# Optimization experiments

Measured on AMD Instinct MI355X. Metric: run time of the kernel, lower is better.

The kernel has to match this reference:

```python
import jax, jax.numpy as jnp
import numpy as np

B, S, DIM = 1, 2048, 2048
NH, NKV, HD = 32, 8, 64
NREP = NH // NKV
SCALE = 1.0 / float(np.sqrt(HD))
NEG = -1e30


def _apply_rope(q, k, rope_cache):
    # q: (B,S,NH,HD), k: (B,S,NKV,HD); rope_cache: (S, HD) = [cos | sin], each HD//2 wide
    cos = rope_cache[:, : HD // 2][None, :, None, :]  # (1,S,1,HD/2)
    sin = rope_cache[:, HD // 2 :][None, :, None, :]

    def rot(x):
        x1, x2 = x[..., : HD // 2], x[..., HD // 2 :]
        return jnp.concatenate([x1 * cos - x2 * sin, x1 * sin + x2 * cos], axis=-1)

    return rot(q), rot(k)


def setup_inputs() -> dict:
    key = jax.random.key(0)
    ks = jax.random.split(key, 12)
    std = 0.02
    x = jax.random.normal(ks[0], (B, S, DIM), jnp.float32)
    # real rotary cos/sin cache
    inv_freq = 1.0 / (10000.0 ** (np.arange(0, HD, 2, dtype=np.float64) / HD))
    freqs = np.outer(np.arange(S, dtype=np.float64), inv_freq)
    rope_cache = jnp.asarray(
        np.concatenate([np.cos(freqs), np.sin(freqs)], axis=-1), jnp.float32
    )  # (S, HD)
    return {
        "x": x,
        "rope_cache": rope_cache,
        "wq_w": jax.random.normal(ks[1], (NH * HD, DIM), jnp.float32) * std,
        "wq_b": jax.random.normal(ks[2], (NH * HD,), jnp.float32) * std,
        "wk_w": jax.random.normal(ks[3], (NKV * HD, DIM), jnp.float32) * std,
        "wk_b": jax.random.normal(ks[4], (NKV * HD,), jnp.float32) * std,
        "wv_w": jax.random.normal(ks[5], (NKV * HD, DIM), jnp.float32) * std,
        "wv_b": jax.random.normal(ks[6], (NKV * HD,), jnp.float32) * std,
        "wo_w": jax.random.normal(ks[7], (DIM, NH * HD), jnp.float32) * std,
        "wo_b": jax.random.normal(ks[8], (DIM,), jnp.float32) * std,
        "sinks": jax.random.normal(ks[9], (NH,), jnp.float32) * std,
    }


def reference(x, rope_cache, wq_w, wq_b, wk_w, wk_b, wv_w, wv_b, wo_w, wo_b, sinks):
    q = (x @ wq_w.T + wq_b).reshape(B, S, NH, HD)
    k = (x @ wk_w.T + wk_b).reshape(B, S, NKV, HD)
    v = (x @ wv_w.T + wv_b).reshape(B, S, NKV, HD)
    q, k = _apply_rope(q, k, rope_cache)
    q = q.transpose(0, 2, 1, 3)  # (B,NH,S,HD)
    k = jnp.repeat(k.transpose(0, 2, 1, 3), NREP, axis=1)  # GQA expand -> (B,NH,S,HD)
    v = jnp.repeat(v.transpose(0, 2, 1, 3), NREP, axis=1)
    scores = jnp.einsum("bhqd,bhkd->bhqk", q, k) * SCALE
    causal = jnp.tril(jnp.ones((S, S), bool))
    scores = jnp.where(causal[None, None], scores, NEG)
    lse = jax.scipy.special.logsumexp(scores, axis=-1)  # (B,NH,S)
    attn = jnp.exp(scores - lse[..., None])
    out = jnp.einsum("bhqk,bhkd->bhqd", attn, v)
    sink_scale = jax.nn.sigmoid(lse - sinks[None, :, None])  # (B,NH,S)
    out = out * sink_scale[..., None]
    out = out.transpose(0, 2, 1, 3).reshape(B, S, NH * HD)
    return out @ wo_w.T + wo_b
```

## Files before the change

### kernel.cpp

```cpp
#include <hip/hip_runtime.h>

typedef unsigned short ushort_t;
typedef short s8v __attribute__((ext_vector_type(8)));
typedef short s4v __attribute__((ext_vector_type(4)));
typedef float f4v __attribute__((ext_vector_type(4)));

#define DIMK   2048
#define NHEAD  32
#define HDIM   64

__device__ __forceinline__ unsigned short f2bf(float f) {
    unsigned u = __float_as_uint(f);
    u += 0x7fffu + ((u >> 16) & 1u);
    return (unsigned short)(u >> 16);
}

__device__ __forceinline__ void gll16(const void* g, void* l) {
    __builtin_amdgcn_global_load_lds(
        (const __attribute__((address_space(1))) void*)g,
        (__attribute__((address_space(3))) void*)l, 16, 0, 0);
}

__device__ __forceinline__ f4v mfma16(s8v a, s8v b, f4v c) {
    return __builtin_amdgcn_mfma_f32_16x16x32_bf16(a, b, c, 0, 0, 0);
}

__global__ __launch_bounds__(256) void cast_all(
    const float* __restrict__ x,  const float* __restrict__ wq,
    const float* __restrict__ wk, const float* __restrict__ wv,
    const float* __restrict__ wo,
    ushort_t* __restrict__ xb,  ushort_t* __restrict__ wqb,
    ushort_t* __restrict__ wkb, ushort_t* __restrict__ wvb,
    ushort_t* __restrict__ wob)
{
    int i = blockIdx.x * 256 + threadIdx.x;
    const float* src; ushort_t* dst;
    if      (i < 1048576) { src = x;  dst = xb; }
    else if (i < 2097152) { src = wq; dst = wqb; i -= 1048576; }
    else if (i < 2359296) { src = wk; dst = wkb; i -= 2097152; }
    else if (i < 2621440) { src = wv; dst = wvb; i -= 2359296; }
    else                  { src = wo; dst = wob; i -= 2621440; }
    float4 v = ((const float4*)src)[i];
    ushort4 o;
    o.x = f2bf(v.x); o.y = f2bf(v.y); o.z = f2bf(v.z); o.w = f2bf(v.w);
    ((ushort4*)dst)[i] = o;
}

__device__ __forceinline__ void gemm_core(
    const ushort_t* __restrict__ A, const ushort_t* __restrict__ Bt,
    int bm, int bn, ushort_t* As, ushort_t* Bs, f4v acc[4][4])
{
    const int tid  = threadIdx.x;
    const int wave = tid >> 6, lane = tid & 63;
    const int c = lane & 15, q4 = lane >> 4;
    const int wm = (wave >> 1) * 64, wn = (wave & 1) * 64;

    const ushort_t* ag = A  + (size_t)(bm * 128 + wave * 32 + (lane >> 2)) * DIMK + (lane & 3) * 8;
    const ushort_t* bg = Bt + (size_t)(bn * 128 + wave * 32 + (lane >> 2)) * DIMK + (lane & 3) * 8;
    ushort_t* as0 = As + (wave * 32) * 32;
    ushort_t* as1 = As + (wave * 32 + 16) * 32;
    ushort_t* bs0 = Bs + (wave * 32) * 32;
    ushort_t* bs1 = Bs + (wave * 32 + 16) * 32;

    for (int k0 = 0; k0 < DIMK; k0 += 32) {
        gll16(ag + k0,             as0);
        gll16(ag + 16 * DIMK + k0, as1);
        gll16(bg + k0,             bs0);
        gll16(bg + 16 * DIMK + k0, bs1);
        __syncthreads();
        s8v af[4], bfv[4];
#pragma unroll
        for (int mt = 0; mt < 4; ++mt)
            af[mt] = *(const s8v*)(As + (wm + mt * 16 + c) * 32 + q4 * 8);
#pragma unroll
        for (int nt = 0; nt < 4; ++nt)
            bfv[nt] = *(const s8v*)(Bs + (wn + nt * 16 + c) * 32 + q4 * 8);
#pragma unroll
        for (int mt = 0; mt < 4; ++mt)
#pragma unroll
            for (int nt = 0; nt < 4; ++nt)
                acc[mt][nt] = mfma16(af[mt], bfv[nt], acc[mt][nt]);
        __syncthreads();
    }
}

__global__ __launch_bounds__(256) void qkv_gemm(
    const ushort_t* __restrict__ Xb,
    const ushort_t* __restrict__ Wqb, const ushort_t* __restrict__ Wkb, const ushort_t* __restrict__ Wvb,
    const float* __restrict__ biasq, const float* __restrict__ biask, const float* __restrict__ biasv,
    const float* __restrict__ rope,
    ushort_t* __restrict__ Qo, ushort_t* __restrict__ Kblk, ushort_t* __restrict__ Vblk)
{
    __shared__ ushort_t As[128 * 32], Bs[128 * 32];
    const int nb = blockIdx.x, bm = blockIdx.y;
    const ushort_t* Bt; const float* bias; int nbl, mode;
    if      (nb < 16) { Bt = Wqb; bias = biasq; nbl = nb;      mode = 0; }
    else if (nb < 20) { Bt = Wkb; bias = biask; nbl = nb - 16; mode = 1; }
    else              { Bt = Wvb; bias = biasv; nbl = nb - 20; mode = 2; }

    const f4v fz = {0.f, 0.f, 0.f, 0.f};
    f4v acc[4][4];
    for (int i = 0; i < 4; ++i) for (int j = 0; j < 4; ++j) acc[i][j] = fz;

    gemm_core(Xb, Bt, bm, nbl, As, Bs, acc);

    const int tid = threadIdx.x, wave = tid >> 6, lane = tid & 63;
    const int c = lane & 15, q4 = lane >> 4;
    const int wm = (wave >> 1) * 64, wn = (wave & 1) * 64;

    if (mode == 0) {
#pragma unroll
        for (int mt = 0; mt < 4; ++mt)
#pragma unroll
            for (int r = 0; r < 4; ++r) {
                int row = bm * 128 + wm + mt * 16 + q4 * 4 + r;
                const float* rp = rope + row * 64;
#pragma unroll
                for (int nt = 0; nt < 2; ++nt) {
                    int col = nbl * 128 + wn + nt * 16 + c;
                    int d   = nt * 16 + c;
                    float cs = rp[d], sn = rp[32 + d];
                    float x1 = acc[mt][nt][r]     + bias[col];
                    float x2 = acc[mt][nt + 2][r] + bias[col + 32];
                    Qo[(size_t)row * 2048 + col]      = f2bf((x1 * cs - x2 * sn) * 0.125f);
                    Qo[(size_t)row * 2048 + col + 32] = f2bf((x1 * sn + x2 * cs) * 0.125f);
                }
            }
    } else if (mode == 1) {
#pragma unroll
        for (int mt = 0; mt < 4; ++mt)
#pragma unroll
            for (int r = 0; r < 4; ++r) {
                int row = bm * 128 + wm + mt * 16 + q4 * 4 + r;
                const float* rp = rope + row * 64;
                int kt = row >> 6, ntk = (row & 63) >> 4, ck = row & 15;
#pragma unroll
                for (int nt = 0; nt < 2; ++nt) {
                    int col = nbl * 128 + wn + nt * 16 + c;
                    int d   = nt * 16 + c;
                    float cs = rp[d], sn = rp[32 + d];
                    float x1 = acc[mt][nt][r]     + bias[col];
                    float x2 = acc[mt][nt + 2][r] + bias[col + 32];
                    float o1 = x1 * cs - x2 * sn;
                    float o2 = x1 * sn + x2 * cs;
                    int kvh = col >> 6;
                    {   int dd = d;       int kc = dd >> 5, q4k = (dd >> 3) & 3, j = dd & 7;
                        Kblk[(((((size_t)kvh * 32 + kt) * 2 + kc) * 4 + ntk) * 64 + q4k * 16 + ck) * 8 + j] = f2bf(o1); }
                    {   int dd = d + 32;  int kc = dd >> 5, q4k = (dd >> 3) & 3, j = dd & 7;
                        Kblk[(((((size_t)kvh * 32 + kt) * 2 + kc) * 4 + ntk) * 64 + q4k * 16 + ck) * 8 + j] = f2bf(o2); }
                }
            }
    } else {
#pragma unroll
        for (int mt = 0; mt < 4; ++mt)
#pragma unroll
            for (int nt = 0; nt < 4; ++nt)
#pragma unroll
                for (int r = 0; r < 4; ++r) {
                    int row = bm * 128 + wm + mt * 16 + q4 * 4 + r;
                    int col = nbl * 128 + wn + nt * 16 + c;
                    int kvh = col >> 6, dcol = col & 63, dt = dcol >> 4, cv = dcol & 15;
                    int kt = row >> 6, K64 = row & 63;
                    int kp = (K64 & 15) * 4 + (K64 >> 4);
                    int kc = kp >> 5, q4v = (kp >> 3) & 3, j = kp & 7;
                    Vblk[(((((size_t)kvh * 32 + kt) * 2 + kc) * 4 + dt) * 64 + q4v * 16 + cv) * 8 + j]
                        = f2bf(acc[mt][nt][r] + bias[col]);
                }
    }
}

__global__ __launch_bounds__(256) void proj_gemm(
    const ushort_t* __restrict__ Ob, const ushort_t* __restrict__ Wob,
    const float* __restrict__ bias, float* __restrict__ Co)
{
    __shared__ ushort_t As[128 * 32], Bs[128 * 32];
    const f4v fz = {0.f, 0.f, 0.f, 0.f};
    f4v acc[4][4];
    for (int i = 0; i < 4; ++i) for (int j = 0; j < 4; ++j) acc[i][j] = fz;

    gemm_core(Ob, Wob, blockIdx.y, blockIdx.x, As, Bs, acc);

    const int tid = threadIdx.x, wave = tid >> 6, lane = tid & 63;
    const int c = lane & 15, q4 = lane >> 4;
    const int wm = (wave >> 1) * 64, wn = (wave & 1) * 64;
#pragma unroll
    for (int mt = 0; mt < 4; ++mt)
#pragma unroll
        for (int nt = 0; nt < 4; ++nt)
#pragma unroll
            for (int r = 0; r < 4; ++r) {
                int row = blockIdx.y * 128 + wm + mt * 16 + q4 * 4 + r;
                int col = blockIdx.x * 128 + wn + nt * 16 + c;
                Co[(size_t)row * 2048 + col] = acc[mt][nt][r] + bias[col];
            }
}

__global__ __launch_bounds__(256) void attn_kernel(
    const ushort_t* __restrict__ Qb,
    const ushort_t* __restrict__ Kblk,
    const ushort_t* __restrict__ Vblk,
    const float* __restrict__ sinks,
    ushort_t* __restrict__ Ob)
{
    __shared__ ushort_t Ps[4][32 * 72];
    const int p = blockIdx.x, h = blockIdx.y, kvh = h >> 2;
    const int tid = threadIdx.x, wave = tid >> 6, lane = tid & 63;
    const int c = lane & 15, q4 = lane >> 4;
    const int t  = (wave < 2) ? p : (31 - p);
    const int q0 = t * 64 + (wave & 1) * 32;
    ushort_t* Pw = &Ps[wave][0];

    s8v qf[2][2];
#pragma unroll
    for (int mi = 0; mi < 2; ++mi)
#pragma unroll
        for (int kc = 0; kc < 2; ++kc)
            qf[mi][kc] = *(const s8v*)(Qb + (size_t)(q0 + mi * 16 + c) * 2048 + h * 64 + kc * 32 + q4 * 8);

    const f4v fz = {0.f, 0.f, 0.f, 0.f};
    f4v Oacc[2][4];
    float Lp[2][4];
#pragma unroll
    for (int mi = 0; mi < 2; ++mi) {
#pragma unroll
        for (int dt = 0; dt < 4; ++dt) Oacc[mi][dt] = fz;
#pragma unroll
        for (int r = 0; r < 4; ++r) Lp[mi][r] = 0.f;
    }

    for (int kt = 0; kt <= t; ++kt) {
        const ushort_t* kp = Kblk + (((size_t)kvh * 32 + kt) * 2) * 4 * 64 * 8;
        const ushort_t* vp = Vblk + (((size_t)kvh * 32 + kt) * 2) * 4 * 64 * 8;
        s8v kf[4][2], vf[4][2];
#pragma unroll
        for (int kc = 0; kc < 2; ++kc)
#pragma unroll
            for (int nt = 0; nt < 4; ++nt)
                kf[nt][kc] = *(const s8v*)(kp + ((kc * 4 + nt) * 64 + lane) * 8);
#pragma unroll
        for (int kc = 0; kc < 2; ++kc)
#pragma unroll
            for (int dt = 0; dt < 4; ++dt)
                vf[dt][kc] = *(const s8v*)(vp + ((kc * 4 + dt) * 64 + lane) * 8);

        f4v S[2][4];
#pragma unroll
        for (int mi = 0; mi < 2; ++mi)
#pragma unroll
            for (int nt = 0; nt < 4; ++nt) S[mi][nt] = fz;
#pragma unroll
        for (int kc = 0; kc < 2; ++kc)
#pragma unroll
            for (int nt = 0; nt < 4; ++nt)
#pragma unroll
                for (int mi = 0; mi < 2; ++mi)
                    S[mi][nt] = mfma16(qf[mi][kc], kf[nt][kc], S[mi][nt]);

        if (kt == t) {
#pragma unroll
            for (int mi = 0; mi < 2; ++mi)
#pragma unroll
                for (int nt = 0; nt < 4; ++nt) {
                    int key = t * 64 + nt * 16 + c;
#pragma unroll
                    for (int r = 0; r < 4; ++r) {
                        int qrow = q0 + mi * 16 + q4 * 4 + r;
                        if (key > qrow) S[mi][nt][r] = -1.0e30f;
                    }
                }
        }

#pragma unroll
        for (int mi = 0; mi < 2; ++mi)
#pragma unroll
            for (int r = 0; r < 4; ++r) {
                s4v pk;
#pragma unroll
                for (int nt = 0; nt < 4; ++nt) {
                    float pv = __expf(S[mi][nt][r]);
                    Lp[mi][r] += pv;
                    pk[nt] = (short)f2bf(pv);
                }
                *(s4v*)(Pw + (mi * 16 + q4 * 4 + r) * 72 + c * 4) = pk;
            }
        s8v pa[2][2];
#pragma unroll
        for (int mi = 0; mi < 2; ++mi)
#pragma unroll
            for (int kc = 0; kc < 2; ++kc)
                pa[mi][kc] = *(const s8v*)(Pw + (mi * 16 + c) * 72 + kc * 32 + q4 * 8);
#pragma unroll
        for (int kc = 0; kc < 2; ++kc)
#pragma unroll
            for (int dt = 0; dt < 4; ++dt)
#pragma unroll
                for (int mi = 0; mi < 2; ++mi)
                    Oacc[mi][dt] = mfma16(pa[mi][kc], vf[dt][kc], Oacc[mi][dt]);
    }

#pragma unroll
    for (int mi = 0; mi < 2; ++mi)
#pragma unroll
        for (int r = 0; r < 4; ++r)
#pragma unroll
            for (int off = 1; off < 16; off <<= 1)
                Lp[mi][r] += __shfl_xor(Lp[mi][r], off);

    const float sk = sinks[h];
#pragma unroll
    for (int mi = 0; mi < 2; ++mi)
#pragma unroll
        for (int r = 0; r < 4; ++r) {
            float L = Lp[mi][r];
            float lse = __logf(L);
            float sig = 1.f / (1.f + __expf(sk - lse));
            float sc  = sig / L;
            int row = q0 + mi * 16 + q4 * 4 + r;
#pragma unroll
            for (int dt = 0; dt < 4; ++dt)
                Ob[(size_t)row * 2048 + h * 64 + dt * 16 + c] = f2bf(Oacc[mi][dt][r] * sc);
        }
}

extern "C" void kernel_launch(void* const* d_in, const int* in_sizes, int n_in,
                              void* d_out, int out_size, void* d_ws, size_t ws_size,
                              hipStream_t stream)
{
    (void)in_sizes; (void)n_in; (void)out_size; (void)ws_size;
    const float* x     = (const float*)d_in[0];
    const float* rope  = (const float*)d_in[1];
    const float* wq    = (const float*)d_in[2];
    const float* qb    = (const float*)d_in[3];
    const float* wk    = (const float*)d_in[4];
    const float* kb    = (const float*)d_in[5];
    const float* wv    = (const float*)d_in[6];
    const float* vb    = (const float*)d_in[7];
    const float* wo    = (const float*)d_in[8];
    const float* wob_f = (const float*)d_in[9];
    const float* sinks = (const float*)d_in[10];
    float* out = (float*)d_out;

    char* ws = (char*)d_ws;
    ushort_t* xb   = (ushort_t*)(ws);
    ushort_t* wqb  = (ushort_t*)(ws + (8ull  << 20));
    ushort_t* wkb  = (ushort_t*)(ws + (16ull << 20));
    ushort_t* wvb  = (ushort_t*)(ws + (18ull << 20));
    ushort_t* wob  = (ushort_t*)(ws + (20ull << 20));
    ushort_t* qo   = (ushort_t*)(ws + (28ull << 20));
    ushort_t* kblk = (ushort_t*)(ws + (36ull << 20));
    ushort_t* vblk = (ushort_t*)(ws + (38ull << 20));
    ushort_t* ao   = (ushort_t*)(ws + (40ull << 20));

    cast_all<<<14336, 256, 0, stream>>>(x, wq, wk, wv, wo, xb, wqb, wkb, wvb, wob);
    qkv_gemm<<<dim3(24, 16), 256, 0, stream>>>(xb, wqb, wkb, wvb, qb, kb, vb, rope, qo, kblk, vblk);
    attn_kernel<<<dim3(16, 32), 256, 0, stream>>>(qo, kblk, vblk, sinks, ao);
    proj_gemm<<<dim3(16, 16), 256, 0, stream>>>(ao, wob, wob_f, out);
}
```

Measured before the change: 247.4 us.

## Shrink GEMM tiles to 128x64, double-buffer attention K/V loads, use exp2 softmax

```diff
diff --git a/kernel.cpp b/kernel.cpp
--- a/kernel.cpp
+++ b/kernel.cpp
@@ -2,17 +2,31 @@
 
 typedef unsigned short ushort_t;
 typedef short s8v __attribute__((ext_vector_type(8)));
-typedef short s4v __attribute__((ext_vector_type(4)));
 typedef float f4v __attribute__((ext_vector_type(4)));
 
 #define DIMK   2048
 #define NHEAD  32
 #define HDIM   64
+#define SCALE_LOG2E 0.18033688f
 
 __device__ __forceinline__ unsigned short f2bf(float f) {
     unsigned u = __float_as_uint(f);
     u += 0x7fffu + ((u >> 16) & 1u);
     return (unsigned short)(u >> 16);
+}
+
+__device__ __forceinline__ unsigned pack_bf2(float f0, float f1) {
+    unsigned a = __float_as_uint(f0) + 0x8000u;
+    unsigned b = __float_as_uint(f1) + 0x8000u;
+    return __builtin_amdgcn_perm(b, a, 0x07060302u);
+}
+
+__device__ __forceinline__ float fexp2(float x) {
+#if __has_builtin(__builtin_amdgcn_exp2f)
+    return __builtin_amdgcn_exp2f(x);
+#else
+    return exp2f(x);
+#endif
 }
 
 __device__ __forceinline__ void gll16(const void* g, void* l) {
@@ -46,37 +60,34 @@
     ((ushort4*)dst)[i] = o;
 }
 
-__device__ __forceinline__ void gemm_core(
+__device__ __forceinline__ void gemm_core64(
     const ushort_t* __restrict__ A, const ushort_t* __restrict__ Bt,
-    int bm, int bn, ushort_t* As, ushort_t* Bs, f4v acc[4][4])
+    int bm, int bn64, ushort_t* As, ushort_t* Bs, f4v acc[2][4])
 {
     const int tid  = threadIdx.x;
     const int wave = tid >> 6, lane = tid & 63;
     const int c = lane & 15, q4 = lane >> 4;
-    const int wm = (wave >> 1) * 64, wn = (wave & 1) * 64;
 
     const ushort_t* ag = A  + (size_t)(bm * 128 + wave * 32 + (lane >> 2)) * DIMK + (lane & 3) * 8;
-    const ushort_t* bg = Bt + (size_t)(bn * 128 + wave * 32 + (lane >> 2)) * DIMK + (lane & 3) * 8;
+    const ushort_t* bg = Bt + (size_t)(bn64 * 64 + wave * 16 + (lane >> 2)) * DIMK + (lane & 3) * 8;
     ushort_t* as0 = As + (wave * 32) * 32;
     ushort_t* as1 = As + (wave * 32 + 16) * 32;
-    ushort_t* bs0 = Bs + (wave * 32) * 32;
-    ushort_t* bs1 = Bs + (wave * 32 + 16) * 32;
+    ushort_t* bs0 = Bs + (wave * 16) * 32;
 
     for (int k0 = 0; k0 < DIMK; k0 += 32) {
         gll16(ag + k0,             as0);
         gll16(ag + 16 * DIMK + k0, as1);
         gll16(bg + k0,             bs0);
-        gll16(bg + 16 * DIMK + k0, bs1);
         __syncthreads();
-        s8v af[4], bfv[4];
-#pragma unroll
-        for (int mt = 0; mt < 4; ++mt)
-            af[mt] = *(const s8v*)(As + (wm + mt * 16 + c) * 32 + q4 * 8);
+        s8v af[2], bfv[4];
+#pragma unroll
+        for (int mt = 0; mt < 2; ++mt)
+            af[mt] = *(const s8v*)(As + (wave * 32 + mt * 16 + c) * 32 + q4 * 8);
 #pragma unroll
         for (int nt = 0; nt < 4; ++nt)
-            bfv[nt] = *(const s8v*)(Bs + (wn + nt * 16 + c) * 32 + q4 * 8);
-#pragma unroll
-        for (int mt = 0; mt < 4; ++mt)
+            bfv[nt] = *(const s8v*)(Bs + (nt * 16 + c) * 32 + q4 * 8);
+#pragma unroll
+        for (int mt = 0; mt < 2; ++mt)
 #pragma unroll
             for (int nt = 0; nt < 4; ++nt)
                 acc[mt][nt] = mfma16(af[mt], bfv[nt], acc[mt][nt]);
@@ -91,79 +102,76 @@
     const float* __restrict__ rope,
     ushort_t* __restrict__ Qo, ushort_t* __restrict__ Kblk, ushort_t* __restrict__ Vblk)
 {
-    __shared__ ushort_t As[128 * 32], Bs[128 * 32];
+    __shared__ ushort_t As[128 * 32], Bs[64 * 32];
     const int nb = blockIdx.x, bm = blockIdx.y;
     const ushort_t* Bt; const float* bias; int nbl, mode;
-    if      (nb < 16) { Bt = Wqb; bias = biasq; nbl = nb;      mode = 0; }
-    else if (nb < 20) { Bt = Wkb; bias = biask; nbl = nb - 16; mode = 1; }
-    else              { Bt = Wvb; bias = biasv; nbl = nb - 20; mode = 2; }
+    if      (nb < 32) { Bt = Wqb; bias = biasq; nbl = nb;      mode = 0; }
+    else if (nb < 40) { Bt = Wkb; bias = biask; nbl = nb - 32; mode = 1; }
+    else              { Bt = Wvb; bias = biasv; nbl = nb - 40; mode = 2; }
 
     const f4v fz = {0.f, 0.f, 0.f, 0.f};
-    f4v acc[4][4];
-    for (int i = 0; i < 4; ++i) for (int j = 0; j < 4; ++j) acc[i][j] = fz;
-
-    gemm_core(Xb, Bt, bm, nbl, As, Bs, acc);
+    f4v acc[2][4];
+    for (int i = 0; i < 2; ++i) for (int j = 0; j < 4; ++j) acc[i][j] = fz;
+
+    gemm_core64(Xb, Bt, bm, nbl, As, Bs, acc);
 
     const int tid = threadIdx.x, wave = tid >> 6, lane = tid & 63;
     const int c = lane & 15, q4 = lane >> 4;
-    const int wm = (wave >> 1) * 64, wn = (wave & 1) * 64;
 
     if (mode == 0) {
 #pragma unroll
-        for (int mt = 0; mt < 4; ++mt)
+        for (int mt = 0; mt < 2; ++mt)
 #pragma unroll
             for (int r = 0; r < 4; ++r) {
-                int row = bm * 128 + wm + mt * 16 + q4 * 4 + r;
+                int row = bm * 128 + wave * 32 + mt * 16 + q4 * 4 + r;
                 const float* rp = rope + row * 64;
 #pragma unroll
                 for (int nt = 0; nt < 2; ++nt) {
-                    int col = nbl * 128 + wn + nt * 16 + c;
                     int d   = nt * 16 + c;
+                    int col = nbl * 64 + d;
                     float cs = rp[d], sn = rp[32 + d];
                     float x1 = acc[mt][nt][r]     + bias[col];
                     float x2 = acc[mt][nt + 2][r] + bias[col + 32];
-                    Qo[(size_t)row * 2048 + col]      = f2bf((x1 * cs - x2 * sn) * 0.125f);
-                    Qo[(size_t)row * 2048 + col + 32] = f2bf((x1 * sn + x2 * cs) * 0.125f);
+                    Qo[(size_t)row * 2048 + col]      = f2bf((x1 * cs - x2 * sn) * SCALE_LOG2E);
+                    Qo[(size_t)row * 2048 + col + 32] = f2bf((x1 * sn + x2 * cs) * SCALE_LOG2E);
                 }
             }
     } else if (mode == 1) {
 #pragma unroll
-        for (int mt = 0; mt < 4; ++mt)
+        for (int mt = 0; mt < 2; ++mt)
 #pragma unroll
             for (int r = 0; r < 4; ++r) {
-                int row = bm * 128 + wm + mt * 16 + q4 * 4 + r;
+                int row = bm * 128 + wave * 32 + mt * 16 + q4 * 4 + r;
                 const float* rp = rope + row * 64;
                 int kt = row >> 6, ntk = (row & 63) >> 4, ck = row & 15;
 #pragma unroll
                 for (int nt = 0; nt < 2; ++nt) {
-                    int col = nbl * 128 + wn + nt * 16 + c;
                     int d   = nt * 16 + c;
+                    int col = nbl * 64 + d;
                     float cs = rp[d], sn = rp[32 + d];
                     float x1 = acc[mt][nt][r]     + bias[col];
                     float x2 = acc[mt][nt + 2][r] + bias[col + 32];
                     float o1 = x1 * cs - x2 * sn;
                     float o2 = x1 * sn + x2 * cs;
-                    int kvh = col >> 6;
                     {   int dd = d;       int kc = dd >> 5, q4k = (dd >> 3) & 3, j = dd & 7;
-                        Kblk[(((((size_t)kvh * 32 + kt) * 2 + kc) * 4 + ntk) * 64 + q4k * 16 + ck) * 8 + j] = f2bf(o1); }
+                        Kblk[(((((size_t)nbl * 32 + kt) * 2 + kc) * 4 + ntk) * 64 + q4k * 16 + ck) * 8 + j] = f2bf(o1); }
                     {   int dd = d + 32;  int kc = dd >> 5, q4k = (dd >> 3) & 3, j = dd & 7;
-                        Kblk[(((((size_t)kvh * 32 + kt) * 2 + kc) * 4 + ntk) * 64 + q4k * 16 + ck) * 8 + j] = f2bf(o2); }
+                        Kblk[(((((size_t)nbl * 32 + kt) * 2 + kc) * 4 + ntk) * 64 + q4k * 16 + ck) * 8 + j] = f2bf(o2); }
                 }
             }
     } else {
 #pragma unroll
-        for (int mt = 0; mt < 4; ++mt)
+        for (int mt = 0; mt < 2; ++mt)
 #pragma unroll
             for (int nt = 0; nt < 4; ++nt)
 #pragma unroll
                 for (int r = 0; r < 4; ++r) {
-                    int row = bm * 128 + wm + mt * 16 + q4 * 4 + r;
-                    int col = nbl * 128 + wn + nt * 16 + c;
-                    int kvh = col >> 6, dcol = col & 63, dt = dcol >> 4, cv = dcol & 15;
+                    int row = bm * 128 + wave * 32 + mt * 16 + q4 * 4 + r;
+                    int col = nbl * 64 + nt * 16 + c;
                     int kt = row >> 6, K64 = row & 63;
                     int kp = (K64 & 15) * 4 + (K64 >> 4);
                     int kc = kp >> 5, q4v = (kp >> 3) & 3, j = kp & 7;
-                    Vblk[(((((size_t)kvh * 32 + kt) * 2 + kc) * 4 + dt) * 64 + q4v * 16 + cv) * 8 + j]
+                    Vblk[(((((size_t)nbl * 32 + kt) * 2 + kc) * 4 + nt) * 64 + q4v * 16 + c) * 8 + j]
                         = f2bf(acc[mt][nt][r] + bias[col]);
                 }
     }
@@ -173,24 +181,23 @@
     const ushort_t* __restrict__ Ob, const ushort_t* __restrict__ Wob,
     const float* __restrict__ bias, float* __restrict__ Co)
 {
-    __shared__ ushort_t As[128 * 32], Bs[128 * 32];
+    __shared__ ushort_t As[128 * 32], Bs[64 * 32];
     const f4v fz = {0.f, 0.f, 0.f, 0.f};
-    f4v acc[4][4];
-    for (int i = 0; i < 4; ++i) for (int j = 0; j < 4; ++j) acc[i][j] = fz;
-
-    gemm_core(Ob, Wob, blockIdx.y, blockIdx.x, As, Bs, acc);
+    f4v acc[2][4];
+    for (int i = 0; i < 2; ++i) for (int j = 0; j < 4; ++j) acc[i][j] = fz;
+
+    gemm_core64(Ob, Wob, blockIdx.y, blockIdx.x, As, Bs, acc);
 
     const int tid = threadIdx.x, wave = tid >> 6, lane = tid & 63;
     const int c = lane & 15, q4 = lane >> 4;
-    const int wm = (wave >> 1) * 64, wn = (wave & 1) * 64;
-#pragma unroll
-    for (int mt = 0; mt < 4; ++mt)
+#pragma unroll
+    for (int mt = 0; mt < 2; ++mt)
 #pragma unroll
         for (int nt = 0; nt < 4; ++nt)
 #pragma unroll
             for (int r = 0; r < 4; ++r) {
-                int row = blockIdx.y * 128 + wm + mt * 16 + q4 * 4 + r;
-                int col = blockIdx.x * 128 + wn + nt * 16 + c;
+                int row = blockIdx.y * 128 + wave * 32 + mt * 16 + q4 * 4 + r;
+                int col = blockIdx.x * 64 + nt * 16 + c;
                 Co[(size_t)row * 2048 + col] = acc[mt][nt][r] + bias[col];
             }
 }
@@ -228,75 +235,99 @@
         for (int r = 0; r < 4; ++r) Lp[mi][r] = 0.f;
     }
 
-    for (int kt = 0; kt <= t; ++kt) {
-        const ushort_t* kp = Kblk + (((size_t)kvh * 32 + kt) * 2) * 4 * 64 * 8;
-        const ushort_t* vp = Vblk + (((size_t)kvh * 32 + kt) * 2) * 4 * 64 * 8;
-        s8v kf[4][2], vf[4][2];
-#pragma unroll
-        for (int kc = 0; kc < 2; ++kc)
-#pragma unroll
-            for (int nt = 0; nt < 4; ++nt)
-                kf[nt][kc] = *(const s8v*)(kp + ((kc * 4 + nt) * 64 + lane) * 8);
-#pragma unroll
-        for (int kc = 0; kc < 2; ++kc)
-#pragma unroll
-            for (int dt = 0; dt < 4; ++dt)
-                vf[dt][kc] = *(const s8v*)(vp + ((kc * 4 + dt) * 64 + lane) * 8);
-
-        f4v S[2][4];
-#pragma unroll
-        for (int mi = 0; mi < 2; ++mi)
-#pragma unroll
-            for (int nt = 0; nt < 4; ++nt) S[mi][nt] = fz;
-#pragma unroll
-        for (int kc = 0; kc < 2; ++kc)
-#pragma unroll
-            for (int nt = 0; nt < 4; ++nt)
-#pragma unroll
-                for (int mi = 0; mi < 2; ++mi)
-                    S[mi][nt] = mfma16(qf[mi][kc], kf[nt][kc], S[mi][nt]);
-
-        if (kt == t) {
-#pragma unroll
-            for (int mi = 0; mi < 2; ++mi)
-#pragma unroll
-                for (int nt = 0; nt < 4; ++nt) {
-                    int key = t * 64 + nt * 16 + c;
-#pragma unroll
-                    for (int r = 0; r < 4; ++r) {
-                        int qrow = q0 + mi * 16 + q4 * 4 + r;
-                        if (key > qrow) S[mi][nt][r] = -1.0e30f;
-                    }
-                }
-        }
-
-#pragma unroll
-        for (int mi = 0; mi < 2; ++mi)
-#pragma unroll
-            for (int r = 0; r < 4; ++r) {
-                s4v pk;
-#pragma unroll
-                for (int nt = 0; nt < 4; ++nt) {
-                    float pv = __expf(S[mi][nt][r]);
-                    Lp[mi][r] += pv;
-                    pk[nt] = (short)f2bf(pv);
-                }
-                *(s4v*)(Pw + (mi * 16 + q4 * 4 + r) * 72 + c * 4) = pk;
-            }
-        s8v pa[2][2];
-#pragma unroll
-        for (int mi = 0; mi < 2; ++mi)
-#pragma unroll
-            for (int kc = 0; kc < 2; ++kc)
-                pa[mi][kc] = *(const s8v*)(Pw + (mi * 16 + c) * 72 + kc * 32 + q4 * 8);
-#pragma unroll
-        for (int kc = 0; kc < 2; ++kc)
-#pragma unroll
-            for (int dt = 0; dt < 4; ++dt)
-#pragma unroll
-                for (int mi = 0; mi < 2; ++mi)
-                    Oacc[mi][dt] = mfma16(pa[mi][kc], vf[dt][kc], Oacc[mi][dt]);
+    const ushort_t* kbase = Kblk + (size_t)kvh * 32 * 4096;
+    const ushort_t* vbase = Vblk + (size_t)kvh * 32 * 4096;
+
+    s8v kfA[4][2], vfA[4][2], kfB[4][2], vfB[4][2];
+
+#define ATTN_PF(KF, VF, KT)                                                      \
+    do {                                                                         \
+        const ushort_t* kp_ = kbase + (size_t)(KT) * 4096;                       \
+        const ushort_t* vp_ = vbase + (size_t)(KT) * 4096;                       \
+        _Pragma("unroll")                                                        \
+        for (int kc = 0; kc < 2; ++kc) {                                         \
+            _Pragma("unroll")                                                    \
+            for (int nt = 0; nt < 4; ++nt) {                                     \
+                KF[nt][kc] = *(const s8v*)(kp_ + ((kc * 4 + nt) * 64 + lane) * 8);\
+                VF[nt][kc] = *(const s8v*)(vp_ + ((kc * 4 + nt) * 64 + lane) * 8);\
+            }                                                                    \
+        }                                                                        \
+    } while (0)
+
+#define ATTN_BODY(KF, VF, KT)                                                    \
+    do {                                                                         \
+        f4v S[2][4];                                                             \
+        _Pragma("unroll")                                                        \
+        for (int mi = 0; mi < 2; ++mi) {                                         \
+            _Pragma("unroll")                                                    \
+            for (int nt = 0; nt < 4; ++nt) S[mi][nt] = fz;                       \
+        }                                                                        \
+        _Pragma("unroll")                                                        \
+        for (int kc = 0; kc < 2; ++kc) {                                         \
+            _Pragma("unroll")                                                    \
+            for (int nt = 0; nt < 4; ++nt) {                                     \
+                _Pragma("unroll")                                                \
+                for (int mi = 0; mi < 2; ++mi)                                   \
+                    S[mi][nt] = mfma16(qf[mi][kc], KF[nt][kc], S[mi][nt]);       \
+            }                                                                    \
+        }                                                                        \
+        if ((KT) == t) {                                                         \
+            _Pragma("unroll")                                                    \
+            for (int mi = 0; mi < 2; ++mi) {                                     \
+                _Pragma("unroll")                                                \
+                for (int nt = 0; nt < 4; ++nt) {                                 \
+                    int key = t * 64 + nt * 16 + c;                              \
+                    _Pragma("unroll")                                            \
+                    for (int r = 0; r < 4; ++r) {                                \
+                        int qrow = q0 + mi * 16 + q4 * 4 + r;                    \
+                        if (key > qrow) S[mi][nt][r] = -1.0e30f;                 \
+                    }                                                            \
+                }                                                                \
+            }                                                                    \
+        }                                                                        \
+        _Pragma("unroll")                                                        \
+        for (int mi = 0; mi < 2; ++mi) {                                         \
+            _Pragma("unroll")                                                    \
+            for (int r = 0; r < 4; ++r) {                                        \
+                float p0 = fexp2(S[mi][0][r]), p1 = fexp2(S[mi][1][r]);          \
+                float p2 = fexp2(S[mi][2][r]), p3 = fexp2(S[mi][3][r]);          \
+                Lp[mi][r] += (p0 + p1) + (p2 + p3);                              \
+                int2 w_; w_.x = (int)pack_bf2(p0, p1); w_.y = (int)pack_bf2(p2, p3); \
+                *(int2*)(Pw + (mi * 16 + q4 * 4 + r) * 72 + c * 4) = w_;         \
+            }                                                                    \
+        }                                                                        \
+        s8v pa[2][2];                                                            \
+        _Pragma("unroll")                                                        \
+        for (int mi = 0; mi < 2; ++mi) {                                         \
+            _Pragma("unroll")                                                    \
+            for (int kc = 0; kc < 2; ++kc)                                       \
+                pa[mi][kc] = *(const s8v*)(Pw + (mi * 16 + c) * 72 + kc * 32 + q4 * 8); \
+        }                                                                        \
+        _Pragma("unroll")                                                        \
+        for (int kc = 0; kc < 2; ++kc) {                                         \
+            _Pragma("unroll")                                                    \
+            for (int dt = 0; dt < 4; ++dt) {                                     \
+                _Pragma("unroll")                                                \
+                for (int mi = 0; mi < 2; ++mi)                                   \
+                    Oacc[mi][dt] = mfma16(pa[mi][kc], VF[dt][kc], Oacc[mi][dt]); \
+            }                                                                    \
+        }                                                                        \
+    } while (0)
+
+    ATTN_PF(kfA, vfA, 0);
+    int kt = 0;
+    while (true) {
+        int n1 = (kt + 1 <= t) ? kt + 1 : t;
+        ATTN_PF(kfB, vfB, n1);
+        ATTN_BODY(kfA, vfA, kt);
+        ++kt; if (kt > t) break;
+        int n2 = (kt + 1 <= t) ? kt + 1 : t;
+        ATTN_PF(kfA, vfA, n2);
+        ATTN_BODY(kfB, vfB, kt);
+        ++kt; if (kt > t) break;
     }
+#undef ATTN_PF
+#undef ATTN_BODY
 
 #pragma unroll
     for (int mi = 0; mi < 2; ++mi)
@@ -352,7 +383,7 @@
     ushort_t* ao   = (ushort_t*)(ws + (40ull << 20));
 
     cast_all<<<14336, 256, 0, stream>>>(x, wq, wk, wv, wo, xb, wqb, wkb, wvb, wob);
-    qkv_gemm<<<dim3(24, 16), 256, 0, stream>>>(xb, wqb, wkb, wvb, qb, kb, vb, rope, qo, kblk, vblk);
+    qkv_gemm<<<dim3(48, 16), 256, 0, stream>>>(xb, wqb, wkb, wvb, qb, kb, vb, rope, qo, kblk, vblk);
     attn_kernel<<<dim3(16, 32), 256, 0, stream>>>(qo, kblk, vblk, sinks, ao);
-    proj_gemm<<<dim3(16, 16), 256, 0, stream>>>(ao, wob, wob_f, out);
-}
+    proj_gemm<<<dim3(32, 16), 256, 0, stream>>>(ao, wob, wob_f, out);
+}
```

Result: slower. 258.5 us (+4.5%).
